# Optimization experiments

Hardware: AMD Instinct MI355X
Metric: run time of the kernel (lower is better)

Reference implementation:

```python
import jax, jax.numpy as jnp
import numpy as np

EMBEDDING_BOUND = 1e4  # uniform init bound for box centers (repo constant)


def setup_inputs() -> dict:
    key = jax.random.key(0)
    k1, k2, k3 = jax.random.split(key, 3)
    num_classes, dim = 100000, 50
    d = dim // 2
    # init per MultiBoxEL.init_embeddings: centers ~ U(-B, B), offsets ~ N(1, 0.333)
    centers = jax.random.uniform(k1, (num_classes, d), dtype=jnp.float32,
                                 minval=-EMBEDDING_BOUND, maxval=EMBEDDING_BOUND)
    offsets = 1.0 + 0.333 * jax.random.normal(k2, (num_classes, d), dtype=jnp.float32)
    class_embeds = jnp.concatenate([centers, offsets], axis=1)  # [C, dim]
    nf1_data = jax.random.randint(k3, (2_000_000, 2), 0, num_classes)  # [N, 2] class ids
    return {"class_embeds": class_embeds, "nf1_data": nf1_data}


def _to_box(emb):
    # get_multiboxes: first half = center, second half = |offsets|
    d = emb.shape[-1] // 2
    return emb[:, :d], jnp.abs(emb[:, d:])


def reference(class_embeds, nf1_data):
    """nf1_loss (C subsumed-by D): batched inclusion loss 1 - Area(C ^ D)/Area(C),
    then L2 norm of relu(losses) over the batch (a scalar), exactly as inclusion_loss."""
    c_emb = class_embeds[nf1_data[:, 0]]  # [N, dim] gather (memory-bound)
    d_emb = class_embeds[nf1_data[:, 1]]
    cc, co = _to_box(c_emb)
    dc, do = _to_box(d_emb)
    # box intersection: [max(lowers), min(uppers)]; empty -> side length clipped to 0
    lo = jnp.maximum(cc - co, dc - do)
    hi = jnp.minimum(cc + co, dc + do)
    inter_area = jnp.prod(jax.nn.relu(hi - lo), axis=-1)  # [N]
    c_area = jnp.prod(2.0 * co, axis=-1)                  # [N] box volume = prod(2*offset)
    loss = jnp.where(c_area == 0, 0.0,
           jnp.where(jnp.isinf(c_area), 1.0 - inter_area / (2.0 * EMBEDDING_BOUND),
                     1.0 - inter_area / c_area))
    return jnp.linalg.norm(jax.nn.relu(loss))
```

## Files before the change

kernel.cpp:

```cpp
#include <hip/hip_runtime.h>
#include <hip/hip_cooperative_groups.h>
#include <math.h>

namespace cg = cooperative_groups;


#define DIMS 25
#define EMB_BOUND 10000.0f
#define PPT 8
#define BLK 512
#define BLK_B 1024
#define TROWS 64
#define TFLOATS (TROWS * 2 * DIMS)
#define FTROWS 128

__global__ void init_ws_kernel(float* ws) {
    if (threadIdx.x == 0 && blockIdx.x == 0) ws[0] = 0.0f;
}

__global__ __launch_bounds__(256, 8) void nf1_fallback_kernel(
    const float* __restrict__ emb, const int2* __restrict__ pairs,
    int n_pairs, float* __restrict__ ws)
{
    const int gl  = threadIdx.x & 31;
    const int gid = blockIdx.x * (blockDim.x >> 5) + (threadIdx.x >> 5);
    const int ngrp = gridDim.x * (blockDim.x >> 5);
    float acc = 0.0f;
    for (int p = gid; p < n_pairs; p += ngrp) {
        int2 pr = pairs[p];
        const float* rc = emb + (size_t)pr.x * (2 * DIMS);
        const float* rd = emb + (size_t)pr.y * (2 * DIMS);
        float t = 1.0f, a = 1.0f;
        if (gl < DIMS) {
            float cc = rc[gl], co = fabsf(rc[DIMS + gl]);
            float dc = rd[gl], dd = fabsf(rd[DIMS + gl]);
            float lo = fmaxf(cc - co, dc - dd);
            float hi = fminf(cc + co, dc + dd);
            t = fmaxf(hi - lo, 0.0f);
            a = 2.0f * co;
        }
        #pragma unroll
        for (int m = 16; m >= 1; m >>= 1) { t *= __shfl_xor(t, m, 32); a *= __shfl_xor(a, m, 32); }
        float loss;
        if (a == 0.0f)     loss = 0.0f;
        else if (isinf(a)) loss = 1.0f - t / (2.0f * EMB_BOUND);
        else               loss = 1.0f - t / a;
        loss = fmaxf(loss, 0.0f);
        if (gl == 0) acc += loss * loss;
    }
    #pragma unroll
    for (int m = 32; m >= 1; m >>= 1) acc += __shfl_xor(acc, m, 64);
    __shared__ float wsum[4];
    if ((threadIdx.x & 63) == 0) wsum[threadIdx.x >> 6] = acc;
    __syncthreads();
    if (threadIdx.x == 0) atomicAdd(ws, wsum[0] + wsum[1] + wsum[2] + wsum[3]);
}

__global__ void fallback_finalize_kernel(const float* __restrict__ ws, float* __restrict__ out) {
    if (threadIdx.x == 0 && blockIdx.x == 0) out[0] = sqrtf(fmaxf(ws[0], 0.0f));
}

__device__ __forceinline__ float slow_pair(const float* __restrict__ emb, int2 pr) {
    const float* ra = emb + (size_t)pr.x * (2 * DIMS);
    const float* rb = emb + (size_t)pr.y * (2 * DIMS);
    float inter = 1.0f, carea = 1.0f;
    for (int j = 0; j < DIMS; j++) {
        float cc = ra[j], co = fabsf(ra[DIMS + j]);
        float dc = rb[j], dd = fabsf(rb[DIMS + j]);
        float lo = fmaxf(cc - co, dc - dd);
        float hi = fminf(cc + co, dc + dd);
        inter *= fmaxf(hi - lo, 0.0f);
        carea *= 2.0f * co;
    }
    float loss;
    if (carea == 0.0f)     loss = 0.0f;
    else if (isinf(carea)) loss = 1.0f - inter / (2.0f * EMB_BOUND);
    else                   loss = 1.0f - inter / carea;
    loss = fmaxf(loss, 0.0f);
    return loss * loss;
}

__device__ __forceinline__ float key_pair(const float2* __restrict__ keys,
                                          const float* __restrict__ emb, int2 pr) {
    float2 ka = keys[pr.x];
    float2 kb = keys[pr.y];
    float t0 = fminf(ka.y, kb.y) - fmaxf(ka.x, kb.x);
    if (t0 > 0.0f) return slow_pair(emb, pr);
    return 1.0f;
}

template <int K>
__device__ __forceinline__ int ring_bucket(float lo, float hi) {
    float w = hi - lo;
    if (w <= 16.0f && fabsf(lo) <= 1.0e6f) {
        int i = (int)floorf(lo * 0.0625f);
        int b = i % K; if (b < 0) b += K;
        return b;
    }
    return K;
}

__device__ __forceinline__ bool ring_pass(unsigned a, unsigned b, unsigned K) {
    unsigned dd = (a >= b) ? (a - b) : (b - a);
    return (a == K) | (b == K) | (dd <= 1u) | (dd == K - 1u);
}

__global__ __launch_bounds__(BLK_B, 1) void fused_kernel(
    const float* __restrict__ emb, float2* __restrict__ keys,
    unsigned char* __restrict__ gbuck,
    const int2* __restrict__ pairs, int n_pairs, int n_rows,
    float* __restrict__ acc, unsigned* __restrict__ ticket,
    float* __restrict__ out)
{
    extern __shared__ unsigned char smem[];
    __shared__ float wsum[BLK_B / 64];

    if (blockIdx.x == 0 && threadIdx.x == 0) { acc[0] = 0.0f; ticket[0] = 0u; }

    {
        float* tile = (float*)smem;
        const int n_tiles = (n_rows + FTROWS - 1) / FTROWS;
        for (int tIdx = blockIdx.x; tIdx < n_tiles; tIdx += gridDim.x) {
            const int r0 = tIdx * FTROWS;
            const int rows = min(FTROWS, n_rows - r0);
            const int cnt = rows * (2 * DIMS);
            const int n4 = cnt >> 2;
            {
                const float4* g4 = (const float4*)(emb + (size_t)r0 * (2 * DIMS));
                float4* s4 = (float4*)tile;
                for (int i = threadIdx.x; i < n4; i += blockDim.x) s4[i] = g4[i];
                for (int i = (n4 << 2) + threadIdx.x; i < cnt; i += blockDim.x)
                    tile[i] = emb[(size_t)r0 * (2 * DIMS) + i];
            }
            __syncthreads();
            if (threadIdx.x < FTROWS && threadIdx.x < rows) {
                const int j = threadIdx.x;
                float c = tile[j * (2 * DIMS)];
                float o = fabsf(tile[j * (2 * DIMS) + DIMS]);
                float lo = c - o, hi = c + o;
                keys[r0 + j] = make_float2(lo, hi);
                gbuck[r0 + j] = (unsigned char)ring_bucket<255>(lo, hi);
            }
            __syncthreads();
        }
    }

    cg::this_grid().sync();

    unsigned char* sbuck = smem;
    {
        const int nb16 = (n_rows + 15) >> 4;
        const uint4* g4 = (const uint4*)gbuck;
        uint4* s4 = (uint4*)sbuck;
        for (int i = threadIdx.x; i < nb16; i += blockDim.x) s4[i] = g4[i];
    }
    __syncthreads();

    const int t = blockIdx.x * blockDim.x + threadIdx.x;
    const int base = t * PPT;

    float sum = 0.0f;
    if (base + PPT - 1 < n_pairs) {
        const int4* p4 = (const int4*)pairs;
        int2 pr[PPT];
        #pragma unroll
        for (int i = 0; i < PPT / 2; i++) {
            int4 q = p4[(PPT / 2) * t + i];
            pr[2 * i]     = make_int2(q.x, q.y);
            pr[2 * i + 1] = make_int2(q.z, q.w);
        }
        unsigned ba[PPT], bb[PPT];
        #pragma unroll
        for (int i = 0; i < PPT; i++) { ba[i] = sbuck[pr[i].x]; bb[i] = sbuck[pr[i].y]; }
        #pragma unroll
        for (int i = 0; i < PPT; i++) {
            if (ring_pass(ba[i], bb[i], 255u)) sum += key_pair(keys, emb, pr[i]);
            else                               sum += 1.0f;
        }
    } else if (base < n_pairs) {
        for (int p = base; p < n_pairs; p++) {
            int2 pr = pairs[p];
            unsigned a = sbuck[pr.x], b = sbuck[pr.y];
            if (ring_pass(a, b, 255u)) sum += key_pair(keys, emb, pr);
            else                       sum += 1.0f;
        }
    }

    #pragma unroll
    for (int m = 32; m >= 1; m >>= 1) sum += __shfl_xor(sum, m, 64);
    if ((threadIdx.x & 63) == 0) wsum[threadIdx.x >> 6] = sum;
    __syncthreads();
    if (threadIdx.x == 0) {
        float s = 0.0f;
        #pragma unroll
        for (int w = 0; w < BLK_B / 64; w++) s += wsum[w];
        atomicAdd(acc, s);
        __threadfence();
        unsigned tk = atomicAdd(ticket, 1u);
        if (tk == gridDim.x - 1) {
            float v = atomicAdd(acc, 0.0f);
            out[0] = sqrtf(fmaxf(v, 0.0f));
        }
    }
}

__global__ __launch_bounds__(256) void repack_byte_kernel(
    const float* __restrict__ emb, float2* __restrict__ keys,
    unsigned char* __restrict__ gbuck,
    float* __restrict__ acc, unsigned* __restrict__ ticket, int n_rows)
{
    __shared__ float tile[TFLOATS];
    if (blockIdx.x == 0 && threadIdx.x == 0) { acc[0] = 0.0f; ticket[0] = 0u; }
    const int n_tiles = (n_rows + TROWS - 1) / TROWS;
    for (int tIdx = blockIdx.x; tIdx < n_tiles; tIdx += gridDim.x) {
        const int r0 = tIdx * TROWS;
        const int rows = min(TROWS, n_rows - r0);
        const int cnt = rows * (2 * DIMS);
        {
            const float4* g4 = (const float4*)(emb + r0 * (2 * DIMS));
            float4* s4 = (float4*)tile;
            const int n4 = cnt >> 2;
            for (int i = threadIdx.x; i < n4; i += blockDim.x) s4[i] = g4[i];
        }
        __syncthreads();
        if (threadIdx.x < TROWS) {
            const int j = threadIdx.x;
            if (j < rows) {
                float c = tile[j * (2 * DIMS)];
                float o = fabsf(tile[j * (2 * DIMS) + DIMS]);
                float lo = c - o, hi = c + o;
                keys[r0 + j] = make_float2(lo, hi);
                gbuck[r0 + j] = (unsigned char)ring_bucket<255>(lo, hi);
            }
        }
        __syncthreads();
    }
}

__global__ __launch_bounds__(BLK_B, 4) void pair_screen_byte_kernel(
    const float2* __restrict__ keys, const unsigned char* __restrict__ gbuck,
    const float* __restrict__ emb, const int2* __restrict__ pairs, int n_pairs,
    int n_rows, float* __restrict__ acc, unsigned* __restrict__ ticket,
    float* __restrict__ out)
{
    extern __shared__ unsigned char sbuck[];
    __shared__ float wsum[BLK_B / 64];
    {
        const int nb16 = (n_rows + 15) >> 4;
        const uint4* g4 = (const uint4*)gbuck;
        uint4* s4 = (uint4*)sbuck;
        for (int i = threadIdx.x; i < nb16; i += blockDim.x) s4[i] = g4[i];
    }
    __syncthreads();

    const int t = blockIdx.x * blockDim.x + threadIdx.x;
    const int base = t * PPT;
    float sum = 0.0f;
    if (base + PPT - 1 < n_pairs) {
        const int4* p4 = (const int4*)pairs;
        int2 pr[PPT];
        #pragma unroll
        for (int i = 0; i < PPT / 2; i++) {
            int4 q = p4[(PPT / 2) * t + i];
            pr[2 * i]     = make_int2(q.x, q.y);
            pr[2 * i + 1] = make_int2(q.z, q.w);
        }
        unsigned ba[PPT], bb[PPT];
        #pragma unroll
        for (int i = 0; i < PPT; i++) { ba[i] = sbuck[pr[i].x]; bb[i] = sbuck[pr[i].y]; }
        #pragma unroll
        for (int i = 0; i < PPT; i++) {
            if (ring_pass(ba[i], bb[i], 255u)) sum += key_pair(keys, emb, pr[i]);
            else                               sum += 1.0f;
        }
    } else if (base < n_pairs) {
        for (int p = base; p < n_pairs; p++) {
            int2 pr = pairs[p];
            unsigned a = sbuck[pr.x], b = sbuck[pr.y];
            if (ring_pass(a, b, 255u)) sum += key_pair(keys, emb, pr);
            else                       sum += 1.0f;
        }
    }

    #pragma unroll
    for (int m = 32; m >= 1; m >>= 1) sum += __shfl_xor(sum, m, 64);
    if ((threadIdx.x & 63) == 0) wsum[threadIdx.x >> 6] = sum;
    __syncthreads();
    if (threadIdx.x == 0) {
        float s = 0.0f;
        #pragma unroll
        for (int w = 0; w < BLK_B / 64; w++) s += wsum[w];
        atomicAdd(acc, s);
        __threadfence();
        unsigned tk = atomicAdd(ticket, 1u);
        if (tk == gridDim.x - 1) {
            float v = atomicAdd(acc, 0.0f);
            out[0] = sqrtf(fmaxf(v, 0.0f));
        }
    }
}

__global__ __launch_bounds__(256) void repack_nib_kernel(
    const float* __restrict__ emb, float2* __restrict__ keys,
    unsigned char* __restrict__ gbuck,
    float* __restrict__ acc, unsigned* __restrict__ ticket, int n_rows)
{
    __shared__ float tile[TFLOATS];
    if (blockIdx.x == 0 && threadIdx.x == 0) { acc[0] = 0.0f; ticket[0] = 0u; }
    const int n_tiles = (n_rows + TROWS - 1) / TROWS;
    for (int tIdx = blockIdx.x; tIdx < n_tiles; tIdx += gridDim.x) {
        const int r0 = tIdx * TROWS;
        const int rows = min(TROWS, n_rows - r0);
        const int cnt = rows * (2 * DIMS);
        {
            const float4* g4 = (const float4*)(emb + r0 * (2 * DIMS));
            float4* s4 = (float4*)tile;
            const int n4 = cnt >> 2;
            for (int i = threadIdx.x; i < n4; i += blockDim.x) s4[i] = g4[i];
        }
        __syncthreads();
        if (threadIdx.x < TROWS) {
            const int j = threadIdx.x;
            int b = 0;
            if (j < rows) {
                float c = tile[j * (2 * DIMS)];
                float o = fabsf(tile[j * (2 * DIMS) + DIMS]);
                float lo = c - o, hi = c + o;
                keys[r0 + j] = make_float2(lo, hi);
                if (o > 300.0f || fabsf(lo) > 1.0e6f) b = 15;
                else {
                    int i600 = (int)floorf(lo * (1.0f / 600.0f));
                    b = ((i600 % 15) + 15) % 15;
                }
            }
            int bhi = __shfl_down(b, 1, 64);
            if ((j & 1) == 0 && j < rows)
                gbuck[(r0 + j) >> 1] = (unsigned char)(b | (bhi << 4));
        }
        __syncthreads();
    }
}

__global__ __launch_bounds__(BLK, 6) void pair_screen_nib_kernel(
    const float2* __restrict__ keys, const unsigned char* __restrict__ gbuck,
    const float* __restrict__ emb, const int2* __restrict__ pairs, int n_pairs,
    int n_rows, float* __restrict__ acc, unsigned* __restrict__ ticket,
    float* __restrict__ out)
{
    __shared__ unsigned char sbuck[50016];
    __shared__ float wsum[BLK / 64];
    {
        const int nb16 = (((n_rows + 1) >> 1) + 15) >> 4;
        const uint4* g4 = (const uint4*)gbuck;
        uint4* s4 = (uint4*)sbuck;
        for (int i = threadIdx.x; i < nb16; i += blockDim.x) s4[i] = g4[i];
    }
    __syncthreads();

    const int t = blockIdx.x * blockDim.x + threadIdx.x;
    const int base = t * PPT;
    float sum = 0.0f;
    if (base + PPT - 1 < n_pairs) {
        const int4* p4 = (const int4*)pairs;
        int2 pr[PPT];
        #pragma unroll
        for (int i = 0; i < PPT / 2; i++) {
            int4 q = p4[(PPT / 2) * t + i];
            pr[2 * i]     = make_int2(q.x, q.y);
            pr[2 * i + 1] = make_int2(q.z, q.w);
        }
        unsigned ba[PPT], bb[PPT];
        #pragma unroll
        for (int i = 0; i < PPT; i++) {
            unsigned va = sbuck[pr[i].x >> 1];
            unsigned vb = sbuck[pr[i].y >> 1];
            ba[i] = ((pr[i].x & 1) ? (va >> 4) : va) & 15u;
            bb[i] = ((pr[i].y & 1) ? (vb >> 4) : vb) & 15u;
        }
        #pragma unroll
        for (int i = 0; i < PPT; i++) {
            if (ring_pass(ba[i], bb[i], 15u)) sum += key_pair(keys, emb, pr[i]);
            else                              sum += 1.0f;
        }
    } else if (base < n_pairs) {
        for (int p = base; p < n_pairs; p++) {
            int2 pr = pairs[p];
            unsigned va = sbuck[pr.x >> 1];
            unsigned vb = sbuck[pr.y >> 1];
            unsigned a = ((pr.x & 1) ? (va >> 4) : va) & 15u;
            unsigned b = ((pr.y & 1) ? (vb >> 4) : vb) & 15u;
            if (ring_pass(a, b, 15u)) sum += key_pair(keys, emb, pr);
            else                      sum += 1.0f;
        }
    }

    #pragma unroll
    for (int m = 32; m >= 1; m >>= 1) sum += __shfl_xor(sum, m, 64);
    if ((threadIdx.x & 63) == 0) wsum[threadIdx.x >> 6] = sum;
    __syncthreads();
    if (threadIdx.x == 0) {
        float s = 0.0f;
        #pragma unroll
        for (int w = 0; w < BLK / 64; w++) s += wsum[w];
        atomicAdd(acc, s);
        __threadfence();
        unsigned tk = atomicAdd(ticket, 1u);
        if (tk == gridDim.x - 1) {
            float v = atomicAdd(acc, 0.0f);
            out[0] = sqrtf(fmaxf(v, 0.0f));
        }
    }
}

extern "C" void kernel_launch(void* const* d_in, const int* in_sizes, int n_in,
                              void* d_out, int out_size, void* d_ws, size_t ws_size,
                              hipStream_t stream) {
    const float* emb  = (const float*)d_in[0];
    const int2*  prs  = (const int2*)d_in[1];
    int n_pairs = in_sizes[1] / 2;
    int n_rows  = in_sizes[0] / (2 * DIMS);

    float*    ws     = (float*)d_ws;
    unsigned* ticket = (unsigned*)(ws + 1);
    float*    out    = (float*)d_out;
    float2*   keys   = (float2*)((char*)d_ws + 256);
    unsigned char* gbuck = (unsigned char*)(keys + n_rows);

    int dev = 0;  hipGetDevice(&dev);
    int maxShared = 0, coop = 0, numCU = 0;
    hipDeviceGetAttribute(&maxShared, hipDeviceAttributeMaxSharedMemoryPerBlock, dev);
    hipDeviceGetAttribute(&coop, hipDeviceAttributeCooperativeLaunch, dev);
    hipDeviceGetAttribute(&numCU, hipDeviceAttributeMultiprocessorCount, dev);

    const size_t tabBytes = (size_t)((n_rows + 15) & ~15);
    const size_t fusedDyn = tabBytes > (size_t)(FTROWS * 2 * DIMS * 4)
                          ? tabBytes : (size_t)(FTROWS * 2 * DIMS * 4);
    const bool ws_ok_byte = (ws_size >= 256 + (size_t)n_rows * 8 + tabBytes + 64) &&
                            ((n_rows & 1) == 0);
    const bool byte_ok = ((size_t)maxShared >= tabBytes + 512) && ws_ok_byte;

    const int threads  = (n_pairs + PPT - 1) / PPT;
    const int sblocks  = (threads + BLK_B - 1) / BLK_B;

    bool launched = false;
    if (byte_ok && coop && ((size_t)maxShared >= fusedDyn + 512)) {
        int blocksPerCU = 0;
        hipError_t oe = hipOccupancyMaxActiveBlocksPerMultiprocessor(
            &blocksPerCU, (const void*)fused_kernel, BLK_B, fusedDyn);
        if (oe == hipSuccess && (long long)blocksPerCU * numCU >= sblocks) {
            void* args[] = { (void*)&emb, (void*)&keys, (void*)&gbuck,
                             (void*)&prs, (void*)&n_pairs, (void*)&n_rows,
                             (void*)&ws, (void*)&ticket, (void*)&out };
            hipError_t le = hipLaunchCooperativeKernel(
                (const void*)fused_kernel, dim3(sblocks), dim3(BLK_B),
                args, (unsigned int)fusedDyn, stream);
            if (le == hipSuccess) launched = true;
        }
    }

    if (!launched && byte_ok) {
        int n_tiles = (n_rows + TROWS - 1) / TROWS;
        hipLaunchKernelGGL(repack_byte_kernel, dim3(min(n_tiles, 1024)), dim3(256), 0, stream,
                           emb, keys, gbuck, ws, ticket, n_rows);
        hipLaunchKernelGGL(pair_screen_byte_kernel, dim3(sblocks), dim3(BLK_B),
                           tabBytes, stream,
                           keys, gbuck, emb, prs, n_pairs, n_rows, ws, ticket, out);
        launched = true;
    }

    if (!launched) {
        const bool nib_ok = (((n_rows + 1) >> 1) <= 50000) && ((n_rows & 1) == 0) &&
                            (ws_size >= 256 + (size_t)n_rows * 8 + ((n_rows + 1) >> 1) + 64);
        if (nib_ok) {
            int n_tiles = (n_rows + TROWS - 1) / TROWS;
            hipLaunchKernelGGL(repack_nib_kernel, dim3(min(n_tiles, 1024)), dim3(256), 0, stream,
                               emb, keys, gbuck, ws, ticket, n_rows);
            int thr = (n_pairs + PPT - 1) / PPT;
            int sb  = (thr + BLK - 1) / BLK;
            hipLaunchKernelGGL(pair_screen_nib_kernel, dim3(sb), dim3(BLK), 0, stream,
                               keys, gbuck, emb, prs, n_pairs, n_rows, ws, ticket, out);
        } else {
            hipLaunchKernelGGL(init_ws_kernel, dim3(1), dim3(64), 0, stream, ws);
            hipLaunchKernelGGL(nf1_fallback_kernel, dim3(4096), dim3(256), 0, stream,
                               emb, prs, n_pairs, ws);
            hipLaunchKernelGGL(fallback_finalize_kernel, dim3(1), dim3(64), 0, stream, ws, out);
        }
    }
}
```

Baseline: 87.53 us.

## Replace bucket-table prefilter and cooperative fused kernel with direct key screening

```diff
diff --git a/kernel.cpp b/kernel.cpp
--- a/kernel.cpp
+++ b/kernel.cpp
@@ -1,18 +1,11 @@
 #include <hip/hip_runtime.h>
-#include <hip/hip_cooperative_groups.h>
 #include <math.h>
-
-namespace cg = cooperative_groups;
 
 
 #define DIMS 25
 #define EMB_BOUND 10000.0f
-#define PPT 8
-#define BLK 512
-#define BLK_B 1024
-#define TROWS 64
-#define TFLOATS (TROWS * 2 * DIMS)
-#define FTROWS 128
+#define PPT 4
+#define SBLK 256
 
 __global__ void init_ws_kernel(float* ws) {
     if (threadIdx.x == 0 && blockIdx.x == 0) ws[0] = 0.0f;
@@ -80,109 +73,60 @@
     return loss * loss;
 }
 
-__device__ __forceinline__ float key_pair(const float2* __restrict__ keys,
-                                          const float* __restrict__ emb, int2 pr) {
-    float2 ka = keys[pr.x];
-    float2 kb = keys[pr.y];
-    float t0 = fminf(ka.y, kb.y) - fmaxf(ka.x, kb.x);
-    if (t0 > 0.0f) return slow_pair(emb, pr);
-    return 1.0f;
+__global__ __launch_bounds__(256) void repack_keys_kernel(
+    const float* __restrict__ emb, float2* __restrict__ keys, int n_rows,
+    float* __restrict__ acc, unsigned* __restrict__ ticket)
+{
+    if (blockIdx.x == 0 && threadIdx.x == 0) { acc[0] = 0.0f; ticket[0] = 0u; }
+    const int r = blockIdx.x * blockDim.x + threadIdx.x;
+    if (r < n_rows) {
+        float c = emb[(size_t)r * (2 * DIMS)];
+        float o = fabsf(emb[(size_t)r * (2 * DIMS) + DIMS]);
+        keys[r] = make_float2(c - o, c + o);
+    }
 }
 
-template <int K>
-__device__ __forceinline__ int ring_bucket(float lo, float hi) {
-    float w = hi - lo;
-    if (w <= 16.0f && fabsf(lo) <= 1.0e6f) {
-        int i = (int)floorf(lo * 0.0625f);
-        int b = i % K; if (b < 0) b += K;
-        return b;
-    }
-    return K;
-}
-
-__device__ __forceinline__ bool ring_pass(unsigned a, unsigned b, unsigned K) {
-    unsigned dd = (a >= b) ? (a - b) : (b - a);
-    return (a == K) | (b == K) | (dd <= 1u) | (dd == K - 1u);
-}
-
-__global__ __launch_bounds__(BLK_B, 1) void fused_kernel(
-    const float* __restrict__ emb, float2* __restrict__ keys,
-    unsigned char* __restrict__ gbuck,
-    const int2* __restrict__ pairs, int n_pairs, int n_rows,
+__global__ __launch_bounds__(SBLK) void pair_screen_direct_kernel(
+    const float2* __restrict__ keys, const float* __restrict__ emb,
+    const int2* __restrict__ pairs, int n_pairs,
     float* __restrict__ acc, unsigned* __restrict__ ticket,
     float* __restrict__ out)
 {
-    extern __shared__ unsigned char smem[];
-    __shared__ float wsum[BLK_B / 64];
-
-    if (blockIdx.x == 0 && threadIdx.x == 0) { acc[0] = 0.0f; ticket[0] = 0u; }
-
-    {
-        float* tile = (float*)smem;
-        const int n_tiles = (n_rows + FTROWS - 1) / FTROWS;
-        for (int tIdx = blockIdx.x; tIdx < n_tiles; tIdx += gridDim.x) {
-            const int r0 = tIdx * FTROWS;
-            const int rows = min(FTROWS, n_rows - r0);
-            const int cnt = rows * (2 * DIMS);
-            const int n4 = cnt >> 2;
-            {
-                const float4* g4 = (const float4*)(emb + (size_t)r0 * (2 * DIMS));
-                float4* s4 = (float4*)tile;
-                for (int i = threadIdx.x; i < n4; i += blockDim.x) s4[i] = g4[i];
-                for (int i = (n4 << 2) + threadIdx.x; i < cnt; i += blockDim.x)
-                    tile[i] = emb[(size_t)r0 * (2 * DIMS) + i];
-            }
-            __syncthreads();
-            if (threadIdx.x < FTROWS && threadIdx.x < rows) {
-                const int j = threadIdx.x;
-                float c = tile[j * (2 * DIMS)];
-                float o = fabsf(tile[j * (2 * DIMS) + DIMS]);
-                float lo = c - o, hi = c + o;
-                keys[r0 + j] = make_float2(lo, hi);
-                gbuck[r0 + j] = (unsigned char)ring_bucket<255>(lo, hi);
-            }
-            __syncthreads();
-        }
-    }
-
-    cg::this_grid().sync();
-
-    unsigned char* sbuck = smem;
-    {
-        const int nb16 = (n_rows + 15) >> 4;
-        const uint4* g4 = (const uint4*)gbuck;
-        uint4* s4 = (uint4*)sbuck;
-        for (int i = threadIdx.x; i < nb16; i += blockDim.x) s4[i] = g4[i];
-    }
-    __syncthreads();
+    __shared__ float wsum[SBLK / 64];
 
     const int t = blockIdx.x * blockDim.x + threadIdx.x;
     const int base = t * PPT;
 
     float sum = 0.0f;
     if (base + PPT - 1 < n_pairs) {
+        int2 pr[PPT];
         const int4* p4 = (const int4*)pairs;
-        int2 pr[PPT];
         #pragma unroll
         for (int i = 0; i < PPT / 2; i++) {
             int4 q = p4[(PPT / 2) * t + i];
             pr[2 * i]     = make_int2(q.x, q.y);
             pr[2 * i + 1] = make_int2(q.z, q.w);
         }
-        unsigned ba[PPT], bb[PPT];
-        #pragma unroll
-        for (int i = 0; i < PPT; i++) { ba[i] = sbuck[pr[i].x]; bb[i] = sbuck[pr[i].y]; }
+        float t0[PPT];
         #pragma unroll
         for (int i = 0; i < PPT; i++) {
-            if (ring_pass(ba[i], bb[i], 255u)) sum += key_pair(keys, emb, pr[i]);
-            else                               sum += 1.0f;
+            float2 ka = keys[pr[i].x];
+            float2 kb = keys[pr[i].y];
+            t0[i] = fminf(ka.y, kb.y) - fmaxf(ka.x, kb.x);
+        }
+        #pragma unroll
+        for (int i = 0; i < PPT; i++) {
+            sum += 1.0f;
+            if (t0[i] > 0.0f) sum += slow_pair(emb, pr[i]) - 1.0f;
         }
     } else if (base < n_pairs) {
         for (int p = base; p < n_pairs; p++) {
             int2 pr = pairs[p];
-            unsigned a = sbuck[pr.x], b = sbuck[pr.y];
-            if (ring_pass(a, b, 255u)) sum += key_pair(keys, emb, pr);
-            else                       sum += 1.0f;
+            float2 ka = keys[pr.x];
+            float2 kb = keys[pr.y];
+            float tt = fminf(ka.y, kb.y) - fmaxf(ka.x, kb.x);
+            if (tt > 0.0f) sum += slow_pair(emb, pr);
+            else           sum += 1.0f;
         }
     }
 
@@ -193,215 +137,7 @@
     if (threadIdx.x == 0) {
         float s = 0.0f;
         #pragma unroll
-        for (int w = 0; w < BLK_B / 64; w++) s += wsum[w];
-        atomicAdd(acc, s);
-        __threadfence();
-        unsigned tk = atomicAdd(ticket, 1u);
-        if (tk == gridDim.x - 1) {
-            float v = atomicAdd(acc, 0.0f);
-            out[0] = sqrtf(fmaxf(v, 0.0f));
-        }
-    }
-}
-
-__global__ __launch_bounds__(256) void repack_byte_kernel(
-    const float* __restrict__ emb, float2* __restrict__ keys,
-    unsigned char* __restrict__ gbuck,
-    float* __restrict__ acc, unsigned* __restrict__ ticket, int n_rows)
-{
-    __shared__ float tile[TFLOATS];
-    if (blockIdx.x == 0 && threadIdx.x == 0) { acc[0] = 0.0f; ticket[0] = 0u; }
-    const int n_tiles = (n_rows + TROWS - 1) / TROWS;
-    for (int tIdx = blockIdx.x; tIdx < n_tiles; tIdx += gridDim.x) {
-        const int r0 = tIdx * TROWS;
-        const int rows = min(TROWS, n_rows - r0);
-        const int cnt = rows * (2 * DIMS);
-        {
-            const float4* g4 = (const float4*)(emb + r0 * (2 * DIMS));
-            float4* s4 = (float4*)tile;
-            const int n4 = cnt >> 2;
-            for (int i = threadIdx.x; i < n4; i += blockDim.x) s4[i] = g4[i];
-        }
-        __syncthreads();
-        if (threadIdx.x < TROWS) {
-            const int j = threadIdx.x;
-            if (j < rows) {
-                float c = tile[j * (2 * DIMS)];
-                float o = fabsf(tile[j * (2 * DIMS) + DIMS]);
-                float lo = c - o, hi = c + o;
-                keys[r0 + j] = make_float2(lo, hi);
-                gbuck[r0 + j] = (unsigned char)ring_bucket<255>(lo, hi);
-            }
-        }
-        __syncthreads();
-    }
-}
-
-__global__ __launch_bounds__(BLK_B, 4) void pair_screen_byte_kernel(
-    const float2* __restrict__ keys, const unsigned char* __restrict__ gbuck,
-    const float* __restrict__ emb, const int2* __restrict__ pairs, int n_pairs,
-    int n_rows, float* __restrict__ acc, unsigned* __restrict__ ticket,
-    float* __restrict__ out)
-{
-    extern __shared__ unsigned char sbuck[];
-    __shared__ float wsum[BLK_B / 64];
-    {
-        const int nb16 = (n_rows + 15) >> 4;
-        const uint4* g4 = (const uint4*)gbuck;
-        uint4* s4 = (uint4*)sbuck;
-        for (int i = threadIdx.x; i < nb16; i += blockDim.x) s4[i] = g4[i];
-    }
-    __syncthreads();
-
-    const int t = blockIdx.x * blockDim.x + threadIdx.x;
-    const int base = t * PPT;
-    float sum = 0.0f;
-    if (base + PPT - 1 < n_pairs) {
-        const int4* p4 = (const int4*)pairs;
-        int2 pr[PPT];
-        #pragma unroll
-        for (int i = 0; i < PPT / 2; i++) {
-            int4 q = p4[(PPT / 2) * t + i];
-            pr[2 * i]     = make_int2(q.x, q.y);
-            pr[2 * i + 1] = make_int2(q.z, q.w);
-        }
-        unsigned ba[PPT], bb[PPT];
-        #pragma unroll
-        for (int i = 0; i < PPT; i++) { ba[i] = sbuck[pr[i].x]; bb[i] = sbuck[pr[i].y]; }
-        #pragma unroll
-        for (int i = 0; i < PPT; i++) {
-            if (ring_pass(ba[i], bb[i], 255u)) sum += key_pair(keys, emb, pr[i]);
-            else                               sum += 1.0f;
-        }
-    } else if (base < n_pairs) {
-        for (int p = base; p < n_pairs; p++) {
-            int2 pr = pairs[p];
-            unsigned a = sbuck[pr.x], b = sbuck[pr.y];
-            if (ring_pass(a, b, 255u)) sum += key_pair(keys, emb, pr);
-            else                       sum += 1.0f;
-        }
-    }
-
-    #pragma unroll
-    for (int m = 32; m >= 1; m >>= 1) sum += __shfl_xor(sum, m, 64);
-    if ((threadIdx.x & 63) == 0) wsum[threadIdx.x >> 6] = sum;
-    __syncthreads();
-    if (threadIdx.x == 0) {
-        float s = 0.0f;
-        #pragma unroll
-        for (int w = 0; w < BLK_B / 64; w++) s += wsum[w];
-        atomicAdd(acc, s);
-        __threadfence();
-        unsigned tk = atomicAdd(ticket, 1u);
-        if (tk == gridDim.x - 1) {
-            float v = atomicAdd(acc, 0.0f);
-            out[0] = sqrtf(fmaxf(v, 0.0f));
-        }
-    }
-}
-
-__global__ __launch_bounds__(256) void repack_nib_kernel(
-    const float* __restrict__ emb, float2* __restrict__ keys,
-    unsigned char* __restrict__ gbuck,
-    float* __restrict__ acc, unsigned* __restrict__ ticket, int n_rows)
-{
-    __shared__ float tile[TFLOATS];
-    if (blockIdx.x == 0 && threadIdx.x == 0) { acc[0] = 0.0f; ticket[0] = 0u; }
-    const int n_tiles = (n_rows + TROWS - 1) / TROWS;
-    for (int tIdx = blockIdx.x; tIdx < n_tiles; tIdx += gridDim.x) {
-        const int r0 = tIdx * TROWS;
-        const int rows = min(TROWS, n_rows - r0);
-        const int cnt = rows * (2 * DIMS);
-        {
-            const float4* g4 = (const float4*)(emb + r0 * (2 * DIMS));
-            float4* s4 = (float4*)tile;
-            const int n4 = cnt >> 2;
-            for (int i = threadIdx.x; i < n4; i += blockDim.x) s4[i] = g4[i];
-        }
-        __syncthreads();
-        if (threadIdx.x < TROWS) {
-            const int j = threadIdx.x;
-            int b = 0;
-            if (j < rows) {
-                float c = tile[j * (2 * DIMS)];
-                float o = fabsf(tile[j * (2 * DIMS) + DIMS]);
-                float lo = c - o, hi = c + o;
-                keys[r0 + j] = make_float2(lo, hi);
-                if (o > 300.0f || fabsf(lo) > 1.0e6f) b = 15;
-                else {
-                    int i600 = (int)floorf(lo * (1.0f / 600.0f));
-                    b = ((i600 % 15) + 15) % 15;
-                }
-            }
-            int bhi = __shfl_down(b, 1, 64);
-            if ((j & 1) == 0 && j < rows)
-                gbuck[(r0 + j) >> 1] = (unsigned char)(b | (bhi << 4));
-        }
-        __syncthreads();
-    }
-}
-
-__global__ __launch_bounds__(BLK, 6) void pair_screen_nib_kernel(
-    const float2* __restrict__ keys, const unsigned char* __restrict__ gbuck,
-    const float* __restrict__ emb, const int2* __restrict__ pairs, int n_pairs,
-    int n_rows, float* __restrict__ acc, unsigned* __restrict__ ticket,
-    float* __restrict__ out)
-{
-    __shared__ unsigned char sbuck[50016];
-    __shared__ float wsum[BLK / 64];
-    {
-        const int nb16 = (((n_rows + 1) >> 1) + 15) >> 4;
-        const uint4* g4 = (const uint4*)gbuck;
-        uint4* s4 = (uint4*)sbuck;
-        for (int i = threadIdx.x; i < nb16; i += blockDim.x) s4[i] = g4[i];
-    }
-    __syncthreads();
-
-    const int t = blockIdx.x * blockDim.x + threadIdx.x;
-    const int base = t * PPT;
-    float sum = 0.0f;
-    if (base + PPT - 1 < n_pairs) {
-        const int4* p4 = (const int4*)pairs;
-        int2 pr[PPT];
-        #pragma unroll
-        for (int i = 0; i < PPT / 2; i++) {
-            int4 q = p4[(PPT / 2) * t + i];
-            pr[2 * i]     = make_int2(q.x, q.y);
-            pr[2 * i + 1] = make_int2(q.z, q.w);
-        }
-        unsigned ba[PPT], bb[PPT];
-        #pragma unroll
-        for (int i = 0; i < PPT; i++) {
-            unsigned va = sbuck[pr[i].x >> 1];
-            unsigned vb = sbuck[pr[i].y >> 1];
-            ba[i] = ((pr[i].x & 1) ? (va >> 4) : va) & 15u;
-            bb[i] = ((pr[i].y & 1) ? (vb >> 4) : vb) & 15u;
-        }
-        #pragma unroll
-        for (int i = 0; i < PPT; i++) {
-            if (ring_pass(ba[i], bb[i], 15u)) sum += key_pair(keys, emb, pr[i]);
-            else                              sum += 1.0f;
-        }
-    } else if (base < n_pairs) {
-        for (int p = base; p < n_pairs; p++) {
-            int2 pr = pairs[p];
-            unsigned va = sbuck[pr.x >> 1];
-            unsigned vb = sbuck[pr.y >> 1];
-            unsigned a = ((pr.x & 1) ? (va >> 4) : va) & 15u;
-            unsigned b = ((pr.y & 1) ? (vb >> 4) : vb) & 15u;
-            if (ring_pass(a, b, 15u)) sum += key_pair(keys, emb, pr);
-            else                      sum += 1.0f;
-        }
-    }
-
-    #pragma unroll
-    for (int m = 32; m >= 1; m >>= 1) sum += __shfl_xor(sum, m, 64);
-    if ((threadIdx.x & 63) == 0) wsum[threadIdx.x >> 6] = sum;
-    __syncthreads();
-    if (threadIdx.x == 0) {
-        float s = 0.0f;
-        #pragma unroll
-        for (int w = 0; w < BLK / 64; w++) s += wsum[w];
+        for (int w = 0; w < SBLK / 64; w++) s += wsum[w];
         atomicAdd(acc, s);
         __threadfence();
         unsigned tk = atomicAdd(ticket, 1u);
@@ -424,66 +160,21 @@
     unsigned* ticket = (unsigned*)(ws + 1);
     float*    out    = (float*)d_out;
     float2*   keys   = (float2*)((char*)d_ws + 256);
-    unsigned char* gbuck = (unsigned char*)(keys + n_rows);
 
-    int dev = 0;  hipGetDevice(&dev);
-    int maxShared = 0, coop = 0, numCU = 0;
-    hipDeviceGetAttribute(&maxShared, hipDeviceAttributeMaxSharedMemoryPerBlock, dev);
-    hipDeviceGetAttribute(&coop, hipDeviceAttributeCooperativeLaunch, dev);
-    hipDeviceGetAttribute(&numCU, hipDeviceAttributeMultiprocessorCount, dev);
+    const bool ws_ok = ws_size >= 256 + (size_t)n_rows * 8 + 64;
 
-    const size_t tabBytes = (size_t)((n_rows + 15) & ~15);
-    const size_t fusedDyn = tabBytes > (size_t)(FTROWS * 2 * DIMS * 4)
-                          ? tabBytes : (size_t)(FTROWS * 2 * DIMS * 4);
-    const bool ws_ok_byte = (ws_size >= 256 + (size_t)n_rows * 8 + tabBytes + 64) &&
-                            ((n_rows & 1) == 0);
-    const bool byte_ok = ((size_t)maxShared >= tabBytes + 512) && ws_ok_byte;
-
-    const int threads  = (n_pairs + PPT - 1) / PPT;
-    const int sblocks  = (threads + BLK_B - 1) / BLK_B;
-
-    bool launched = false;
-    if (byte_ok && coop && ((size_t)maxShared >= fusedDyn + 512)) {
-        int blocksPerCU = 0;
-        hipError_t oe = hipOccupancyMaxActiveBlocksPerMultiprocessor(
-            &blocksPerCU, (const void*)fused_kernel, BLK_B, fusedDyn);
-        if (oe == hipSuccess && (long long)blocksPerCU * numCU >= sblocks) {
-            void* args[] = { (void*)&emb, (void*)&keys, (void*)&gbuck,
-                             (void*)&prs, (void*)&n_pairs, (void*)&n_rows,
-                             (void*)&ws, (void*)&ticket, (void*)&out };
-            hipError_t le = hipLaunchCooperativeKernel(
-                (const void*)fused_kernel, dim3(sblocks), dim3(BLK_B),
-                args, (unsigned int)fusedDyn, stream);
-            if (le == hipSuccess) launched = true;
-        }
-    }
-
-    if (!launched && byte_ok) {
-        int n_tiles = (n_rows + TROWS - 1) / TROWS;
-        hipLaunchKernelGGL(repack_byte_kernel, dim3(min(n_tiles, 1024)), dim3(256), 0, stream,
-                           emb, keys, gbuck, ws, ticket, n_rows);
-        hipLaunchKernelGGL(pair_screen_byte_kernel, dim3(sblocks), dim3(BLK_B),
-                           tabBytes, stream,
-                           keys, gbuck, emb, prs, n_pairs, n_rows, ws, ticket, out);
-        launched = true;
-    }
-
-    if (!launched) {
-        const bool nib_ok = (((n_rows + 1) >> 1) <= 50000) && ((n_rows & 1) == 0) &&
-                            (ws_size >= 256 + (size_t)n_rows * 8 + ((n_rows + 1) >> 1) + 64);
-        if (nib_ok) {
-            int n_tiles = (n_rows + TROWS - 1) / TROWS;
-            hipLaunchKernelGGL(repack_nib_kernel, dim3(min(n_tiles, 1024)), dim3(256), 0, stream,
-                               emb, keys, gbuck, ws, ticket, n_rows);
-            int thr = (n_pairs + PPT - 1) / PPT;
-            int sb  = (thr + BLK - 1) / BLK;
-            hipLaunchKernelGGL(pair_screen_nib_kernel, dim3(sb), dim3(BLK), 0, stream,
-                               keys, gbuck, emb, prs, n_pairs, n_rows, ws, ticket, out);
-        } else {
-            hipLaunchKernelGGL(init_ws_kernel, dim3(1), dim3(64), 0, stream, ws);
-            hipLaunchKernelGGL(nf1_fallback_kernel, dim3(4096), dim3(256), 0, stream,
-                               emb, prs, n_pairs, ws);
-            hipLaunchKernelGGL(fallback_finalize_kernel, dim3(1), dim3(64), 0, stream, ws, out);
-        }
+    if (ws_ok) {
+        const int rblocks = (n_rows + 255) / 256;
+        hipLaunchKernelGGL(repack_keys_kernel, dim3(rblocks), dim3(256), 0, stream,
+                           emb, keys, n_rows, ws, ticket);
+        const int threads = (n_pairs + PPT - 1) / PPT;
+        const int sblocks = (threads + SBLK - 1) / SBLK;
+        hipLaunchKernelGGL(pair_screen_direct_kernel, dim3(sblocks), dim3(SBLK), 0, stream,
+                           keys, emb, prs, n_pairs, ws, ticket, out);
+    } else {
+        hipLaunchKernelGGL(init_ws_kernel, dim3(1), dim3(64), 0, stream, ws);
+        hipLaunchKernelGGL(nf1_fallback_kernel, dim3(4096), dim3(256), 0, stream,
+                           emb, prs, n_pairs, ws);
+        hipLaunchKernelGGL(fallback_finalize_kernel, dim3(1), dim3(64), 0, stream, ws, out);
     }
 }
```

Result: slower. 142.6 us (+62.9%).
